# Performance work log

Hardware: AMD Instinct MI355X
Metric: run time of the kernel (lower is better)

Reference implementation:

```python
import jax, jax.numpy as jnp
import numpy as np

B, S, H = 2, 512, 768
E, M, R, R2 = 64, 64, 128, 128
NER_C, REL_C, SIZE_E, CLS = 10, 8, 32, 101
NEG = -1e30


def _linear(x, w, b):
    # torch nn.Linear convention: w is [out, in]
    return x @ w.T + b


def _span_pool(emb, masks):
    # emb [B,S,H], masks [B,K,S] -> masked max over tokens -> [B,K,H]
    neg = jnp.where(masks[..., None] != 0, 0.0, NEG)  # [B,K,S,1]
    return jnp.max(neg + emb[:, None, :, :], axis=2)


def _classify_spans(input_ids, emb, masks, size_emb, rep_w, rep_b, head_w, head_b):
    pool = _span_pool(emb, masks)                      # [B,K,H]
    cls_idx = jnp.argmax((input_ids == CLS).astype(jnp.int32), axis=1)
    ctx = emb[jnp.arange(emb.shape[0]), cls_idx]       # [B,H] (get_token)
    rep = jnp.concatenate([jnp.broadcast_to(ctx[:, None, :], pool.shape), pool, size_emb], axis=-1)
    clf = _linear(jax.nn.relu(_linear(rep, rep_w, rep_b)), head_w, head_b)
    return clf, pool


def _classify_relations(pool, size_emb, rels, rel_masks, emb, w1, b1, w2, b2, w3, b3):
    Bc = pool.shape[0]
    bidx = jnp.arange(Bc)[:, None, None]
    pairs = pool[bidx, rels].reshape(Bc, rels.shape[1], -1)        # [B,R,2H]
    size_pairs = size_emb[bidx, rels].reshape(Bc, rels.shape[1], -1)  # [B,R,2*SIZE_E]
    # masked max over context tokens (rel mask)
    ctx = jnp.max(jnp.where(rel_masks[..., None] != 0, 0.0, NEG) + emb[:, None, :, :], axis=2)
    ctx = jnp.where(jnp.any(rel_masks != 0, axis=-1)[..., None], ctx, 0.0)
    rel_repr = jnp.concatenate([ctx, pairs, size_pairs], axis=-1)  # [B,R,3H+2*SIZE_E]
    h = jax.nn.relu(_linear(rel_repr, w1, b1))
    h = jax.nn.relu(_linear(h, w2, b2))
    return _linear(h, w3, b3)


def setup_inputs():
    key = jax.random.key(0)
    ks = jax.random.split(key, 24)
    p = lambda k, shape: jax.random.normal(k, shape, jnp.float32) * 0.02
    ids = jax.random.randint(ks[0], (B, S), 2000, 30000)
    ids = ids.at[:, 0].set(CLS)  # exactly one cls token per row
    return dict(
        input_ids=ids,
        entity_masks=jax.random.randint(ks[1], (B, E, S), 0, 2).astype(jnp.int32),
        entity_sizes=jax.random.randint(ks[2], (B, E), 0, 100),
        mention_masks=jax.random.randint(ks[3], (B, M, S), 0, 2).astype(jnp.int32),
        mention_sizes=jax.random.randint(ks[4], (B, M), 0, 100),
        relations=jax.random.randint(ks[5], (B, R, 2), 0, E),
        rel_masks=jax.random.randint(ks[6], (B, R, S), 0, 2).astype(jnp.int32),
        references=jax.random.randint(ks[7], (B, R2, 2), 0, M),
        references_masks=jax.random.randint(ks[8], (B, R2, S), 0, 2).astype(jnp.int32),
        token_embedding=jax.random.normal(ks[9], (B, S, H), jnp.float32),
        ner_size_emb=p(ks[10], (100, SIZE_E)),
        emd_size_emb=p(ks[11], (100, SIZE_E)),
        ner_rep_w=p(ks[12], (H, 2 * H + SIZE_E)), ner_rep_b=jnp.zeros(H, jnp.float32),
        ner_head_w=p(ks[13], (NER_C, H)), ner_head_b=jnp.zeros(NER_C, jnp.float32),
        emd_rep_w=p(ks[14], (H, 2 * H + SIZE_E)), emd_rep_b=jnp.zeros(H, jnp.float32),
        emd_head_w=p(ks[15], (2, H)), emd_head_b=jnp.zeros(2, jnp.float32),
        rel_w1=p(ks[16], (H, 3 * H + 2 * SIZE_E)), rel_b1=jnp.zeros(H, jnp.float32),
        rel_w2=p(ks[17], (H, H)), rel_b2=jnp.zeros(H, jnp.float32),
        rel_w3=p(ks[18], (REL_C, H)), rel_b3=jnp.zeros(REL_C, jnp.float32),
        cr_w1=p(ks[19], (H, 3 * H + 2 * SIZE_E)), cr_b1=jnp.zeros(H, jnp.float32),
        cr_w2=p(ks[20], (H, H)), cr_b2=jnp.zeros(H, jnp.float32),
        cr_w3=p(ks[21], (1, H)), cr_b3=jnp.zeros(1, jnp.float32),
    )


def reference(input_ids, entity_masks, entity_sizes, mention_masks, mention_sizes,
              relations, rel_masks, references, references_masks, token_embedding,
              ner_size_emb, emd_size_emb,
              ner_rep_w, ner_rep_b, ner_head_w, ner_head_b,
              emd_rep_w, emd_rep_b, emd_head_w, emd_head_b,
              rel_w1, rel_b1, rel_w2, rel_b2, rel_w3, rel_b3,
              cr_w1, cr_b1, cr_w2, cr_b2, cr_w3, cr_b3):
    sz = ner_size_emb[entity_sizes]                                    # [B,E,SIZE_E]
    entity_clf, entity_pool = _classify_spans(input_ids, token_embedding, entity_masks, sz,
                                              ner_rep_w, ner_rep_b, ner_head_w, ner_head_b)
    rel_clf = _classify_relations(entity_pool, sz, relations, rel_masks, token_embedding,
                                  rel_w1, rel_b1, rel_w2, rel_b2, rel_w3, rel_b3)
    msz = emd_size_emb[mention_sizes]
    mention_clf, mention_pool = _classify_spans(input_ids, token_embedding, mention_masks, msz,
                                                emd_rep_w, emd_rep_b, emd_head_w, emd_head_b)
    ref_clf = _classify_relations(mention_pool, msz, references, references_masks, token_embedding,
                                  cr_w1, cr_b1, cr_w2, cr_b2, cr_w3, cr_b3)
    return entity_clf, rel_clf, mention_clf, ref_clf
```

## Files before the change

kernel.cpp:

```cpp
#include <hip/hip_runtime.h>
#include <hip/hip_bf16.h>

typedef __hip_bfloat16 bf16;
typedef __attribute__((ext_vector_type(8))) short short8;
typedef __attribute__((ext_vector_type(4))) float f32x4;

#define SS 512
#define HD 768
#define NEGC (-1e30f)
#define NSPLIT 16
#define TOK 32
#define POOL_BLOCKS 1536
#define D1_BLOCKS (POOL_BLOCKS + 4)

__device__ __forceinline__ short8 cvt8(float4 a, float4 b)
{
  union { bf16 h[8]; short8 s; } u;
  u.h[0] = __hip_bfloat16(a.x); u.h[1] = __hip_bfloat16(a.y);
  u.h[2] = __hip_bfloat16(a.z); u.h[3] = __hip_bfloat16(a.w);
  u.h[4] = __hip_bfloat16(b.x); u.h[5] = __hip_bfloat16(b.y);
  u.h[6] = __hip_bfloat16(b.z); u.h[7] = __hip_bfloat16(b.w);
  return u.s;
}

__global__ __launch_bounds__(256) void k_d1(
    const int* __restrict__ e_masks, const int* __restrict__ m_masks,
    const int* __restrict__ r_masks, const int* __restrict__ c_masks,
    const float* __restrict__ emb, const int* __restrict__ input_ids,
    const int* __restrict__ esizes, const int* __restrict__ msizes,
    const float* __restrict__ nsemb, const float* __restrict__ esemb,
    bf16* __restrict__ part, int* __restrict__ flags,
    bf16* __restrict__ sze, bf16* __restrict__ szm,
    bf16* __restrict__ ctxb, float* __restrict__ out)
{
  int bx = blockIdx.x;
  int t  = threadIdx.x;

  if (bx >= POOL_BLOCKS) {
    int q = bx - POOL_BLOCKS;
    if (q == 0) {
      for (int i = t; i < 128 * 32; i += 256)
        sze[i] = __hip_bfloat16(nsemb[(size_t)esizes[i >> 5] * 32 + (i & 31)]);
    } else if (q == 1) {
      for (int i = t; i < 128 * 32; i += 256)
        szm[i] = __hip_bfloat16(esemb[(size_t)msizes[i >> 5] * 32 + (i & 31)]);
    } else if (q == 2) {
      __shared__ int s_cls;
      for (int b2 = 0; b2 < 2; b2++) {
        if (t == 0) s_cls = SS;
        __syncthreads();
        for (int s = t; s < SS; s += 256)
          if (input_ids[b2 * SS + s] == 101) atomicMin(&s_cls, s);
        __syncthreads();
        int ci = (s_cls == SS) ? 0 : s_cls;
        for (int hh = t; hh < HD; hh += 256)
          ctxb[(size_t)b2 * HD + hh] = __hip_bfloat16(emb[((size_t)b2 * SS + ci) * HD + hh]);
        __syncthreads();
      }
    } else {
      for (int i = t; i < 3840; i += 256) out[i] = 0.f;
    }
    return;
  }

  int g  = bx % 48;
  int b  = (bx / 48) & 1;
  int sp = bx / 96;
  int j0 = g * 8;

  const int* marr; int row0;
  if      (j0 < 64)  { marr = e_masks; row0 = b*64  +  j0;        }
  else if (j0 < 128) { marr = m_masks; row0 = b*64  + (j0-64);    }
  else if (j0 < 256) { marr = r_masks; row0 = b*128 + (j0-128);   }
  else               { marr = c_masks; row0 = b*128 + (j0-256);   }

  __shared__ unsigned s_pack[TOK];
  __shared__ unsigned s_any;
  if (t == 0) s_any = 0u;
  __syncthreads();

  int sbase = sp * TOK;
  if (t < TOK) {
    unsigned w = 0;
    #pragma unroll
    for (int k = 0; k < 8; k++) {
      int mm = marr[(size_t)(row0 + k) * SS + sbase + t];
      w |= (mm != 0 ? 1u : 0u) << k;
    }
    s_pack[t] = w;
    atomicOr(&s_any, w);
  }
  __syncthreads();

  float a0[8], a1[8], a2[8];
  #pragma unroll
  for (int k = 0; k < 8; k++) { a0[k] = -INFINITY; a1[k] = -INFINITY; a2[k] = -INFINITY; }

  const float* ep = emb + ((size_t)b * SS + sbase) * HD + t * 3;
  #pragma unroll 2
  for (int s = 0; s < TOK; s++) {
    float v0 = ep[0];
    float v1 = ep[1];
    float v2 = ep[2];
    ep += HD;
    unsigned wm = s_pack[s];
    #pragma unroll
    for (int k = 0; k < 8; k++) {
      float add = (wm & (1u << k)) ? 0.f : NEGC;
      a0[k] = fmaxf(a0[k], v0 + add);
      a1[k] = fmaxf(a1[k], v1 + add);
      a2[k] = fmaxf(a2[k], v2 + add);
    }
  }

  #pragma unroll
  for (int k = 0; k < 8; k++) {
    int sg = b * 384 + j0 + k;
    bf16* dst = part + ((size_t)sp * 768 + sg) * HD + t * 3;
    dst[0] = __hip_bfloat16(a0[k]);
    dst[1] = __hip_bfloat16(a1[k]);
    dst[2] = __hip_bfloat16(a2[k]);
  }
  if (t < 8) flags[sp * 768 + b * 384 + j0 + t] = (int)((s_any >> t) & 1u);
}

__global__ __launch_bounds__(256) void k_combine(
    const bf16* __restrict__ part, const int* __restrict__ flags,
    bf16* __restrict__ epool, bf16* __restrict__ mpool,
    bf16* __restrict__ rctx, bf16* __restrict__ cctx)
{
  int sg = blockIdx.x;
  int b = sg / 384, j = sg % 384;
  int any = 0;
  #pragma unroll
  for (int sp = 0; sp < NSPLIT; sp++) any |= flags[sp * 768 + sg];

  int h = threadIdx.x * 3;
  float v0 = -INFINITY, v1 = -INFINITY, v2 = -INFINITY;
  #pragma unroll
  for (int sp = 0; sp < NSPLIT; sp++) {
    const bf16* src = part + ((size_t)sp * 768 + sg) * HD + h;
    v0 = fmaxf(v0, (float)src[0]);
    v1 = fmaxf(v1, (float)src[1]);
    v2 = fmaxf(v2, (float)src[2]);
  }
  bf16* dst;
  if      (j < 64)  { dst = epool + ((size_t)b*64  + j)       * HD + h; }
  else if (j < 128) { dst = mpool + ((size_t)b*64  + (j-64))  * HD + h; }
  else if (j < 256) { dst = rctx  + ((size_t)b*128 + (j-128)) * HD + h;
                      if (!any) { v0 = 0.f; v1 = 0.f; v2 = 0.f; } }
  else              { dst = cctx  + ((size_t)b*128 + (j-256)) * HD + h;
                      if (!any) { v0 = 0.f; v1 = 0.f; v2 = 0.f; } }
  dst[0] = __hip_bfloat16(v0);
  dst[1] = __hip_bfloat16(v1);
  dst[2] = __hip_bfloat16(v2);
}

struct P1 {
  const bf16 *ctx, *pool, *sz; const int* ridx;
  const float* W; const float* bias;
  bf16* C;
  const float *hw, *hb; float* outp;
  int is_rel, N, K, Mtiles;
};
struct P1x4 { P1 p[4]; };

__global__ __launch_bounds__(256, 2) void k_gemm1(P1x4 args)
{
  P1 g = args.p[blockIdx.z];
  int x = blockIdx.x;
  if (x >= g.Mtiles) return;
  int mt = x * 32, nt = blockIdx.y * 32;
  int wave = threadIdx.x >> 6, lane = threadIdx.x & 63;
  int lm = lane & 15, quad = lane >> 4;
  int K_ = g.K;

  const bf16 *g0[2], *g1[2], *g2[2], *g3[2], *g4[2];
  int rr[2] = { mt + lm, mt + 16 + lm };
  #pragma unroll
  for (int i = 0; i < 2; i++) {
    int r = rr[i];
    if (g.is_rel) {
      int b = r >> 7;
      int i0 = g.ridx[2 * r], i1 = g.ridx[2 * r + 1];
      g0[i] = g.ctx  + (size_t)r * HD;
      g1[i] = g.pool + (size_t)(b * 64 + i0) * HD;
      g2[i] = g.pool + (size_t)(b * 64 + i1) * HD;
      g3[i] = g.sz   + (size_t)(b * 64 + i0) * 32;
      g4[i] = g.sz   + (size_t)(b * 64 + i1) * 32;
    } else {
      g0[i] = g.ctx  + (size_t)(r >> 6) * HD;
      g1[i] = g.pool + (size_t)r * HD;
      g2[i] = g.sz   + (size_t)r * 32;
      g3[i] = g2[i]; g4[i] = g2[i];
    }
  }
  const float* w0p = g.W + (size_t)(nt + lm)      * K_ + quad * 8;
  const float* w1p = g.W + (size_t)(nt + 16 + lm) * K_ + quad * 8;

  f32x4 acc00 = {0.f,0.f,0.f,0.f}, acc01 = {0.f,0.f,0.f,0.f};
  f32x4 acc10 = {0.f,0.f,0.f,0.f}, acc11 = {0.f,0.f,0.f,0.f};

  for (int k32 = wave * 32; k32 < K_; k32 += 128) {
    const bf16 *b0, *b1;
    if      (k32 < 768)  { b0 = g0[0] + k32;          b1 = g0[1] + k32;          }
    else if (k32 < 1536) { b0 = g1[0] + (k32 - 768);  b1 = g1[1] + (k32 - 768);  }
    else if (k32 < 2304) { b0 = g2[0] + (k32 - 1536); b1 = g2[1] + (k32 - 1536); }
    else if (k32 < 2336) { b0 = g3[0] + (k32 - 2304); b1 = g3[1] + (k32 - 2304); }
    else                 { b0 = g4[0] + (k32 - 2336); b1 = g4[1] + (k32 - 2336); }
    short8 a0 = *(const short8*)((const short*)b0 + quad * 8);
    short8 a1 = *(const short8*)((const short*)b1 + quad * 8);
    const float* wq0 = w0p + k32;
    const float* wq1 = w1p + k32;
    short8 w0 = cvt8(*(const float4*)wq0, *(const float4*)(wq0 + 4));
    short8 w1 = cvt8(*(const float4*)wq1, *(const float4*)(wq1 + 4));
    acc00 = __builtin_amdgcn_mfma_f32_16x16x32_bf16(a0, w0, acc00, 0, 0, 0);
    acc01 = __builtin_amdgcn_mfma_f32_16x16x32_bf16(a0, w1, acc01, 0, 0, 0);
    acc10 = __builtin_amdgcn_mfma_f32_16x16x32_bf16(a1, w0, acc10, 0, 0, 0);
    acc11 = __builtin_amdgcn_mfma_f32_16x16x32_bf16(a1, w1, acc11, 0, 0, 0);
  }

  __shared__ float smem[4 * 32 * 32];
  #pragma unroll
  for (int reg = 0; reg < 4; reg++) {
    int r = quad * 4 + reg;
    smem[wave*1024 + r*32 + lm]             = acc00[reg];
    smem[wave*1024 + r*32 + 16 + lm]        = acc01[reg];
    smem[wave*1024 + (16 + r)*32 + lm]      = acc10[reg];
    smem[wave*1024 + (16 + r)*32 + 16 + lm] = acc11[reg];
  }
  __syncthreads();

  int c = threadIdx.x & 31;
  int rb = threadIdx.x >> 5;
  float bb = g.bias[nt + c];
  #pragma unroll
  for (int i = 0; i < 4; i++) {
    int r = rb + 8 * i;
    float v = smem[r*32 + c] + smem[1024 + r*32 + c] + smem[2048 + r*32 + c] + smem[3072 + r*32 + c];
    v = fmaxf(v + bb, 0.f);
    if (g.C) g.C[(size_t)(mt + r) * HD + nt + c] = __hip_bfloat16(v);
    else     smem[r*32 + c] = v;
  }
  __syncthreads();

  if (!g.C) {
    int r = threadIdx.x >> 3, oi = threadIdx.x & 7;
    for (int o = oi; o < g.N; o += 8) {
      float s = 0.f;
      #pragma unroll
      for (int cc = 0; cc < 32; cc++) {
        int c2 = (cc + r) & 31;
        s += smem[r*32 + c2] * g.hw[(size_t)o * HD + nt + c2];
      }
      if (blockIdx.y == 0) s += g.hb[o];
      atomicAdd(g.outp + (size_t)(mt + r) * g.N + o, s);
    }
  }
}

struct P2 { const short* A; const float* W; const float* bias;
            const float *hw, *hb; float* outp; int N; };
struct P2x2 { P2 p[2]; };

__global__ __launch_bounds__(256, 2) void k_gemm2(P2x2 args)
{
  P2 g = args.p[blockIdx.z];
  int mt = blockIdx.x * 32, nt = blockIdx.y * 32;
  int wave = threadIdx.x >> 6, lane = threadIdx.x & 63;
  int lm = lane & 15, quad = lane >> 4;

  const short* a0p = g.A + (size_t)(mt + lm)      * HD + quad * 8;
  const short* a1p = g.A + (size_t)(mt + 16 + lm) * HD + quad * 8;
  const float* w0p = g.W + (size_t)(nt + lm)      * HD + quad * 8;
  const float* w1p = g.W + (size_t)(nt + 16 + lm) * HD + quad * 8;

  f32x4 acc00 = {0.f,0.f,0.f,0.f}, acc01 = {0.f,0.f,0.f,0.f};
  f32x4 acc10 = {0.f,0.f,0.f,0.f}, acc11 = {0.f,0.f,0.f,0.f};

  for (int k32 = wave * 32; k32 < HD; k32 += 128) {
    short8 a0 = *(const short8*)(a0p + k32);
    short8 a1 = *(const short8*)(a1p + k32);
    short8 w0 = cvt8(*(const float4*)(w0p + k32), *(const float4*)(w0p + k32 + 4));
    short8 w1 = cvt8(*(const float4*)(w1p + k32), *(const float4*)(w1p + k32 + 4));
    acc00 = __builtin_amdgcn_mfma_f32_16x16x32_bf16(a0, w0, acc00, 0, 0, 0);
    acc01 = __builtin_amdgcn_mfma_f32_16x16x32_bf16(a0, w1, acc01, 0, 0, 0);
    acc10 = __builtin_amdgcn_mfma_f32_16x16x32_bf16(a1, w0, acc10, 0, 0, 0);
    acc11 = __builtin_amdgcn_mfma_f32_16x16x32_bf16(a1, w1, acc11, 0, 0, 0);
  }

  __shared__ float smem[4 * 32 * 32];
  #pragma unroll
  for (int reg = 0; reg < 4; reg++) {
    int r = quad * 4 + reg;
    smem[wave*1024 + r*32 + lm]             = acc00[reg];
    smem[wave*1024 + r*32 + 16 + lm]        = acc01[reg];
    smem[wave*1024 + (16 + r)*32 + lm]      = acc10[reg];
    smem[wave*1024 + (16 + r)*32 + 16 + lm] = acc11[reg];
  }
  __syncthreads();

  int c = threadIdx.x & 31;
  int rb = threadIdx.x >> 5;
  float bb = g.bias[nt + c];
  #pragma unroll
  for (int i = 0; i < 4; i++) {
    int r = rb + 8 * i;
    float v = smem[r*32 + c] + smem[1024 + r*32 + c] + smem[2048 + r*32 + c] + smem[3072 + r*32 + c];
    smem[r*32 + c] = fmaxf(v + bb, 0.f);
  }
  __syncthreads();

  int r = threadIdx.x >> 3, oi = threadIdx.x & 7;
  for (int o = oi; o < g.N; o += 8) {
    float s = 0.f;
    #pragma unroll
    for (int cc = 0; cc < 32; cc++) {
      int c2 = (cc + r) & 31;
      s += smem[r*32 + c2] * g.hw[(size_t)o * HD + nt + c2];
    }
    if (blockIdx.y == 0) s += g.hb[o];
    atomicAdd(g.outp + (size_t)(mt + r) * g.N + o, s);
  }
}

extern "C" void kernel_launch(void* const* d_in, const int* in_sizes, int n_in,
                              void* d_out, int out_size, void* d_ws, size_t ws_size,
                              hipStream_t stream)
{
  const int*   input_ids  = (const int*)d_in[0];
  const int*   e_masks    = (const int*)d_in[1];
  const int*   e_sizes    = (const int*)d_in[2];
  const int*   m_masks    = (const int*)d_in[3];
  const int*   m_sizes    = (const int*)d_in[4];
  const int*   relations  = (const int*)d_in[5];
  const int*   r_masks    = (const int*)d_in[6];
  const int*   references = (const int*)d_in[7];
  const int*   c_masks    = (const int*)d_in[8];
  const float* emb        = (const float*)d_in[9];
  const float* nsemb      = (const float*)d_in[10];
  const float* esemb      = (const float*)d_in[11];
  const float* ner_rep_w  = (const float*)d_in[12];
  const float* ner_rep_b  = (const float*)d_in[13];
  const float* ner_head_w = (const float*)d_in[14];
  const float* ner_head_b = (const float*)d_in[15];
  const float* emd_rep_w  = (const float*)d_in[16];
  const float* emd_rep_b  = (const float*)d_in[17];
  const float* emd_head_w = (const float*)d_in[18];
  const float* emd_head_b = (const float*)d_in[19];
  const float* rel_w1 = (const float*)d_in[20];
  const float* rel_b1 = (const float*)d_in[21];
  const float* rel_w2 = (const float*)d_in[22];
  const float* rel_b2 = (const float*)d_in[23];
  const float* rel_w3 = (const float*)d_in[24];
  const float* rel_b3 = (const float*)d_in[25];
  const float* cr_w1 = (const float*)d_in[26];
  const float* cr_b1 = (const float*)d_in[27];
  const float* cr_w2 = (const float*)d_in[28];
  const float* cr_b2 = (const float*)d_in[29];
  const float* cr_w3 = (const float*)d_in[30];
  const float* cr_b3 = (const float*)d_in[31];
  float* out = (float*)d_out;

  bf16* wsb = (bf16*)d_ws;
  size_t ob = 0;
  bf16* PART  = wsb + ob; ob += (size_t)NSPLIT * 768 * HD;
  bf16* EPOOL = wsb + ob; ob += (size_t)128 * HD;
  bf16* MPOOL = wsb + ob; ob += (size_t)128 * HD;
  bf16* RCTX  = wsb + ob; ob += (size_t)256 * HD;
  bf16* CCTX  = wsb + ob; ob += (size_t)256 * HD;
  bf16* SZE   = wsb + ob; ob += (size_t)128 * 32;
  bf16* SZM   = wsb + ob; ob += (size_t)128 * 32;
  bf16* CTXB  = wsb + ob; ob += (size_t)2 * HD;
  bf16* RH1   = wsb + ob; ob += (size_t)256 * HD;
  bf16* CH1   = wsb + ob; ob += (size_t)256 * HD;
  int*  FLAGS = (int*)(wsb + ob); ob += (size_t)2 * NSPLIT * 768;

  k_d1<<<D1_BLOCKS, 256, 0, stream>>>(
      e_masks, m_masks, r_masks, c_masks, emb, input_ids,
      e_sizes, m_sizes, nsemb, esemb,
      PART, FLAGS, SZE, SZM, CTXB, out);

  k_combine<<<768, 256, 0, stream>>>(PART, FLAGS, EPOOL, MPOOL, RCTX, CCTX);

  P1x4 a1;
  a1.p[0] = { CTXB, EPOOL, SZE, nullptr,    ner_rep_w, ner_rep_b,
              nullptr, ner_head_w, ner_head_b, out,        0, 10, 1568, 4 };
  a1.p[1] = { CTXB, MPOOL, SZM, nullptr,    emd_rep_w, emd_rep_b,
              nullptr, emd_head_w, emd_head_b, out + 3328, 0, 2,  1568, 4 };
  a1.p[2] = { RCTX, EPOOL, SZE, relations,  rel_w1, rel_b1,
              RH1, nullptr, nullptr, nullptr,              1, 0,  2368, 8 };
  a1.p[3] = { CCTX, MPOOL, SZM, references, cr_w1, cr_b1,
              CH1, nullptr, nullptr, nullptr,              1, 0,  2368, 8 };
  k_gemm1<<<dim3(8, 24, 4), 256, 0, stream>>>(a1);

  P2x2 a2;
  a2.p[0] = { (const short*)RH1, rel_w2, rel_b2, rel_w3, rel_b3, out + 1280, 8 };
  a2.p[1] = { (const short*)CH1, cr_w2,  cr_b2,  cr_w3,  cr_b3,  out + 3584, 1 };
  k_gemm2<<<dim3(8, 24, 2), 256, 0, stream>>>(a2);
}
```

Measured before the change: 206.8 us.

## Halve pooling split count, unroll token loop by two, reorder partials by span

The span max-pool kernel now splits the sequence into 8 chunks of 64 tokens instead of 16 of 32. That halves the pooling block count and the bf16 partial traffic the combine kernel has to read. The token loop handles two tokens per step and moves the mask words into scalar registers with readfirstlane. Partial and flag buffers are re-laid out span-major so each span's splits sit next to each other. In exchange, fewer blocks means less parallelism, and each block runs a longer serial loop.

```diff
diff --git a/kernel.cpp b/kernel.cpp
--- a/kernel.cpp
+++ b/kernel.cpp
@@ -8,9 +8,9 @@
 #define SS 512
 #define HD 768
 #define NEGC (-1e30f)
-#define NSPLIT 16
-#define TOK 32
-#define POOL_BLOCKS 1536
+#define NSPLIT 8
+#define TOK 64
+#define POOL_BLOCKS 768
 #define D1_BLOCKS (POOL_BLOCKS + 4)
 
 __device__ __forceinline__ short8 cvt8(float4 a, float4 b)
@@ -98,30 +98,35 @@
 
   const float* ep = emb + ((size_t)b * SS + sbase) * HD + t * 3;
   #pragma unroll 2
-  for (int s = 0; s < TOK; s++) {
-    float v0 = ep[0];
-    float v1 = ep[1];
-    float v2 = ep[2];
-    ep += HD;
-    unsigned wm = s_pack[s];
+  for (int s = 0; s < TOK; s += 2) {
+    float u0 = ep[0];
+    float u1 = ep[1];
+    float u2 = ep[2];
+    float v0 = ep[HD];
+    float v1 = ep[HD + 1];
+    float v2 = ep[HD + 2];
+    ep += 2 * HD;
+    unsigned w0 = (unsigned)__builtin_amdgcn_readfirstlane((int)s_pack[s]);
+    unsigned w1 = (unsigned)__builtin_amdgcn_readfirstlane((int)s_pack[s + 1]);
     #pragma unroll
     for (int k = 0; k < 8; k++) {
-      float add = (wm & (1u << k)) ? 0.f : NEGC;
-      a0[k] = fmaxf(a0[k], v0 + add);
-      a1[k] = fmaxf(a1[k], v1 + add);
-      a2[k] = fmaxf(a2[k], v2 + add);
+      float add0 = (w0 & (1u << k)) ? 0.f : NEGC;
+      float add1 = (w1 & (1u << k)) ? 0.f : NEGC;
+      a0[k] = fmaxf(fmaxf(a0[k], u0 + add0), v0 + add1);
+      a1[k] = fmaxf(fmaxf(a1[k], u1 + add0), v1 + add1);
+      a2[k] = fmaxf(fmaxf(a2[k], u2 + add0), v2 + add1);
     }
   }
 
   #pragma unroll
   for (int k = 0; k < 8; k++) {
     int sg = b * 384 + j0 + k;
-    bf16* dst = part + ((size_t)sp * 768 + sg) * HD + t * 3;
+    bf16* dst = part + ((size_t)sg * NSPLIT + sp) * HD + t * 3;
     dst[0] = __hip_bfloat16(a0[k]);
     dst[1] = __hip_bfloat16(a1[k]);
     dst[2] = __hip_bfloat16(a2[k]);
   }
-  if (t < 8) flags[sp * 768 + b * 384 + j0 + t] = (int)((s_any >> t) & 1u);
+  if (t < 8) flags[(size_t)(b * 384 + j0 + t) * NSPLIT + sp] = (int)((s_any >> t) & 1u);
 }
 
 __global__ __launch_bounds__(256) void k_combine(
@@ -133,13 +138,13 @@
   int b = sg / 384, j = sg % 384;
   int any = 0;
   #pragma unroll
-  for (int sp = 0; sp < NSPLIT; sp++) any |= flags[sp * 768 + sg];
+  for (int sp = 0; sp < NSPLIT; sp++) any |= flags[(size_t)sg * NSPLIT + sp];
 
   int h = threadIdx.x * 3;
   float v0 = -INFINITY, v1 = -INFINITY, v2 = -INFINITY;
   #pragma unroll
   for (int sp = 0; sp < NSPLIT; sp++) {
-    const bf16* src = part + ((size_t)sp * 768 + sg) * HD + h;
+    const bf16* src = part + ((size_t)sg * NSPLIT + sp) * HD + h;
     v0 = fmaxf(v0, (float)src[0]);
     v1 = fmaxf(v1, (float)src[1]);
     v2 = fmaxf(v2, (float)src[2]);
```

Measured after the change: 207.3 us. About the same (+0.2%).
